# Kernel optimization log

Measured on AMD Instinct MI355X. Metric: run time of the kernel, lower is better.

The kernel has to match this reference:

```python
import jax, jax.numpy as jnp
import numpy as np

N_NODES = 50000
EPS_NORM = 1e-12
EPS_ENT = 1e-8

def _l2norm(x):
    # torch.nn.functional.normalize: x / clamp(||x||, min=1e-12)
    n = jnp.sqrt(jnp.sum(x * x, axis=-1, keepdims=True))
    return x / jnp.maximum(n, EPS_NORM)

def _layer(hidden, src, dst, edge_type, multi_emb, proto_emb):
    # hidden: [N,H]; multi_emb: [R,P,H]; proto_emb: [P,H]
    inp_j = hidden[src]                          # [E,H] gather
    rel_basis = multi_emb[edge_type]             # [E,P,H] gather
    sims = jnp.einsum('eh,ph->ep', _l2norm(inp_j), _l2norm(proto_emb))  # cosine sim [E,P]
    proto_proba = jax.nn.softmax(sims, axis=1)   # [E,P]
    msg = jnp.einsum('ep,eph->eh', proto_proba, rel_basis)              # [E,H]
    ent = -jnp.sum(proto_proba * jnp.log(proto_proba + EPS_ENT), axis=1)  # [E]
    logits = -ent
    # scatter_softmax over destination index
    seg_max = jax.ops.segment_max(logits, dst, num_segments=N_NODES)
    ex = jnp.exp(logits - seg_max[dst])
    denom = jax.ops.segment_sum(ex, dst, num_segments=N_NODES)
    attn = ex / denom[dst]                       # [E]
    out = jax.ops.segment_sum(attn[:, None] * msg, dst, num_segments=N_NODES)  # [N,H]
    return out

def setup_inputs() -> dict:
    key = jax.random.key(0)
    ks = jax.random.split(key, 6)
    E = 800000
    H, R, P, L = 128, 18, 18, 3  # num_layers=4 -> 3 NBFCluttr layers
    edge_index = jax.random.randint(ks[0], (2, E), 0, N_NODES, dtype=jnp.int64) if jax.config.read('jax_enable_x64') else jax.random.randint(ks[0], (2, E), 0, N_NODES, dtype=jnp.int32)
    edge_type = jax.random.randint(ks[1], (E,), 0, R, dtype=edge_index.dtype)
    tail_indices = jax.random.randint(ks[2], (1024,), 0, N_NODES, dtype=edge_index.dtype)
    multi_embeddings = jax.random.uniform(ks[3], (L, R, P, H), dtype=jnp.float32)
    proto_embeddings = jax.random.uniform(ks[4], (L, P, H), dtype=jnp.float32)
    source_embedding = jax.random.uniform(ks[5], (H,), dtype=jnp.float32)
    return {"edge_index": edge_index, "edge_type": edge_type, "tail_indices": tail_indices,
            "multi_embeddings": multi_embeddings, "proto_embeddings": proto_embeddings,
            "source_embedding": source_embedding}

def reference(edge_index, edge_type, tail_indices, multi_embeddings, proto_embeddings, source_embedding):
    src, dst = edge_index[0], edge_index[1]
    H = source_embedding.shape[0]
    # boundary condition: source node gets source_embedding, rest zero
    hidden = jnp.zeros((N_NODES, H), dtype=source_embedding.dtype).at[0].set(source_embedding)
    L = multi_embeddings.shape[0]
    for l in range(L):  # small fixed loop over structurally distinct layers
        hidden = _layer(hidden, src, dst, edge_type, multi_embeddings[l], proto_embeddings[l])
    # apply_classifier, eval_mode=True, use_mlp_classifier=False -> cosine sims to last layer prototypes
    out_emb = hidden[tail_indices]               # [B,H]
    sims = jnp.einsum('nh,ph->np', _l2norm(out_emb), _l2norm(proto_embeddings[-1]))
    return sims  # gumbel_softmax_sample with eval_mode=True returns logits unchanged
```

## Files before the change

### kernel.cpp

```cpp
#include <hip/hip_runtime.h>
#include <hip/hip_bf16.h>


#define N_NODES 50000
#define H 128
#define P 18
#define RP 324
#define KPAD 352
#define K0PAD 64
#define ELLW 64
#define NPART 8
#define NODES_PER_PART 6250

typedef _Float16 half8 __attribute__((ext_vector_type(8)));
typedef float floatx4 __attribute__((ext_vector_type(4)));

__global__ __launch_bounds__(256) void zero_u32_kernel(unsigned* p, int n) {
  int i = blockIdx.x * 256 + threadIdx.x;
  if (i < n) p[i] = 0u;
}

__global__ __launch_bounds__(256) void ell_kernel(const int* __restrict__ src,
                                                  const int* __restrict__ dst,
                                                  const int* __restrict__ etype,
                                                  unsigned* __restrict__ cur,
                                                  unsigned* __restrict__ ep, int E) {
  int part = blockIdx.x & (NPART - 1);
  int i = (blockIdx.x >> 3) * 256 + threadIdx.x;
  if (i >= E) return;
  int d = dst[i];
  int lo = part * NODES_PER_PART;
  if (d < lo || d >= lo + NODES_PER_PART) return;
  unsigned pos = atomicAdd(&cur[d], 1u);
  if (pos < ELLW)
    ep[(size_t)d * ELLW + pos] = (unsigned)src[i] | ((unsigned)etype[i] << 20);
}

__global__ __launch_bounds__(64) void protoq0_kernel(const float* __restrict__ proto,
                                                     const float* __restrict__ semb,
                                                     float* __restrict__ pN,
                                                     float* __restrict__ q0r) {
  int row = blockIdx.x, l = threadIdx.x;
  if (row < 54) {
    float a = proto[row * H + l], b = proto[row * H + 64 + l];
    float ss = a * a + b * b;
    for (int m = 32; m > 0; m >>= 1) ss += __shfl_xor(ss, m, 64);
    float inv = 1.f / fmaxf(sqrtf(ss), 1e-12f);
    pN[row * H + l] = a * inv;
    pN[row * H + 64 + l] = b * inv;
    return;
  }
  float s0 = semb[l], s1 = semb[l + 64];
  float ss = s0 * s0 + s1 * s1;
  float dot[P];
#pragma unroll
  for (int p = 0; p < P; p++) {
    float a = proto[p * H + l], b = proto[p * H + 64 + l];
    float rn = a * a + b * b;
    for (int m = 32; m > 0; m >>= 1) rn += __shfl_xor(rn, m, 64);
    float rinv = 1.f / fmaxf(sqrtf(rn), 1e-12f);
    dot[p] = (s0 * a + s1 * b) * rinv;
  }
  for (int m = 1; m <= 32; m <<= 1) {
    ss += __shfl_xor(ss, m, 64);
#pragma unroll
    for (int p = 0; p < P; p++) dot[p] += __shfl_xor(dot[p], m, 64);
  }
  float inv = 1.f / fmaxf(sqrtf(ss), 1e-12f);
  float sum = 0.f;
#pragma unroll
  for (int p = 0; p < P; p++) {
    dot[p] = __expf(dot[p] * inv - 1.f);
    sum += dot[p];
  }
  float isum = 1.f / sum, ent = 0.f;
#pragma unroll
  for (int p = 0; p < P; p++) {
    dot[p] *= isum;
    ent -= dot[p] * __logf(dot[p] + 1e-8f);
  }
  float w = __expf(-ent);
  if (l < P) q0r[l] = w * dot[l];
}

__global__ __launch_bounds__(256) void bprep_kernel(const float* __restrict__ multi,
                                                    const float* __restrict__ q0r,
                                                    _Float16* __restrict__ Btg,
                                                    _Float16* __restrict__ Btl0) {
  int idx = blockIdx.x * 256 + threadIdx.x;
  if (idx < 2 * H * KPAD) {
    int l = idx / (H * KPAD), rem = idx - l * (H * KPAD);
    int h = rem / KPAD, k = rem - h * KPAD;
    const float* B = multi + (size_t)(l + 1) * RP * H;
    Btg[idx] = (k < RP) ? (_Float16)B[k * H + h] : (_Float16)0.f;
    return;
  }
  int idx2 = idx - 2 * H * KPAD;
  if (idx2 >= H * K0PAD) return;
  int h = idx2 >> 6, k = idx2 & 63;
  float pr = 1.f / 18.f, ent = 0.f;
#pragma unroll
  for (int p = 0; p < P; p++) ent -= pr * __logf(pr + 1e-8f);
  float qc = __expf(-ent) * pr;
  float v = 0.f;
  if (k < P) {
#pragma unroll
    for (int p = 0; p < P; p++) v += qc * multi[(k * P + p) * H + h];
  } else if (k < 2 * P) {
    int r = k - P;
#pragma unroll
    for (int p = 0; p < P; p++) v += (q0r[p] - qc) * multi[(r * P + p) * H + h];
  }
  Btl0[h * K0PAD + k] = (_Float16)v;
}

__global__ __launch_bounds__(256) void hist_kernel(const unsigned* __restrict__ ep,
                                                   const unsigned* __restrict__ cur,
                                                   _Float16* __restrict__ M, int n) {
  int wave = threadIdx.x >> 6, lane = threadIdx.x & 63;
  int nd = blockIdx.x * 4 + wave;
  if (nd >= n) return;
  int cnt = (int)cur[nd];
  if (cnt > ELLW) cnt = ELLW;
  bool a = lane < cnt;
  unsigned pk = a ? ep[(size_t)nd * ELLW + lane] : 0xFFFFFFFFu;
  int r = (int)(pk >> 20);
  unsigned long long zm = __ballot(a && (pk & 0xFFFFFu) == 0u);
  float creg = 0.f, creg0 = 0.f;
#pragma unroll
  for (int rr = 0; rr < P; rr++) {
    unsigned long long m = __ballot(a && (r == rr));
    if (lane == rr) {
      creg = (float)__popcll(m);
      creg0 = (float)__popcll(m & zm);
    }
  }
  int slx = (lane >= P && lane < 2 * P) ? lane - P : 0;
  float v0 = __shfl(creg0, slx, 64);
  float val = (lane < P) ? creg : ((lane < 2 * P) ? v0 : 0.f);
  M[(size_t)nd * K0PAD + lane] = (_Float16)val;
}

__global__ __launch_bounds__(256) void scatter_kernel(const unsigned* __restrict__ ep,
                                                      const unsigned* __restrict__ cur,
                                                      const float* __restrict__ q,
                                                      const int* __restrict__ tl,
                                                      _Float16* __restrict__ M, int n) {
  __shared__ float sl[4][3 * RP];
  int wave = threadIdx.x >> 6, lane = threadIdx.x & 63;
  int t = blockIdx.x * 4 + wave;
  float* s0 = sl[wave];
  for (int i = lane; i < 3 * RP; i += 64) s0[i] = 0.f;
  int sub = lane / 18;
  int j = lane - sub * 18;
  bool act = (sub < 3) && (t < n);
  int cnt = 0;
  size_t b = 0;
  if (t < n) {
    int nd = tl ? tl[t] : t;
    b = (size_t)nd * ELLW;
    cnt = (int)cur[nd];
    if (cnt > ELLW) cnt = ELLW;
  }
  float* ms = s0 + (sub < 3 ? sub : 0) * RP;
  for (int it = 0; it < cnt; it += 9) {
    bool a0 = act && (it + sub < cnt);
    bool a1 = act && (it + 3 + sub < cnt);
    bool a2 = act && (it + 6 + sub < cnt);
    unsigned pk0 = 0, pk1 = 0, pk2 = 0;
    if (a0) pk0 = ep[b + it + sub];
    if (a1) pk1 = ep[b + it + 3 + sub];
    if (a2) pk2 = ep[b + it + 6 + sub];
    float q0 = 0.f, q1 = 0.f, q2 = 0.f;
    if (a0) q0 = q[(size_t)(pk0 & 0xFFFFFu) * P + j];
    if (a1) q1 = q[(size_t)(pk1 & 0xFFFFFu) * P + j];
    if (a2) q2 = q[(size_t)(pk2 & 0xFFFFFu) * P + j];
    if (a0) ms[(pk0 >> 20) * P + j] += q0;
    if (a1) ms[(pk1 >> 20) * P + j] += q1;
    if (a2) ms[(pk2 >> 20) * P + j] += q2;
  }
  if (t < n) {
    for (int k = lane; k < RP; k += 64)
      M[(size_t)t * KPAD + k] = (_Float16)(s0[k] + s0[RP + k] + s0[2 * RP + k]);
    for (int k = RP + lane; k < KPAD; k += 64) M[(size_t)t * KPAD + k] = (_Float16)0.f;
  }
}

template <int MODE>
__global__ __launch_bounds__(256) void gemm_kernel(const _Float16* __restrict__ M,
                                                   const _Float16* __restrict__ Bt,
                                                   const float* __restrict__ pN,
                                                   float* __restrict__ q_out, int n,
                                                   int kpad) {
  __shared__ float smem_f[64 * 132];
  _Float16* As = (_Float16*)smem_f;
  _Float16* Bs = (_Float16*)(smem_f + 1024);
  int tid = threadIdx.x;
  int wave = tid >> 6, lane = tid & 63;
  int m15 = lane & 15, quad = lane >> 4;
  int n0 = blockIdx.x * 64;
  floatx4 acc[4][2] = {};

  __shared__ float pns[4 * P * 36];
  for (int i = tid; i < 4 * P * 32; i += 256) {
    int s = i / (P * 32), r = i - s * (P * 32);
    int p = r >> 5, kk = r & 31;
    pns[s * (P * 36) + p * 36 + kk] = pN[p * H + s * 32 + kk];
  }

  for (int kt = 0; kt < (kpad >> 5); kt++) {
    int k0 = kt * 32;
    __syncthreads();
    {
      int row = tid >> 2, kc = (tid & 3) * 8;
      int gr = n0 + row;
      half8 v = {};
      if (gr < n) v = *(const half8*)(M + (size_t)gr * kpad + k0 + kc);
      *(half8*)(As + row * 32 + kc) = v;
    }
    {
      int col = tid >> 1, kc = (tid & 1) * 16;
      const _Float16* srcp = Bt + (size_t)col * kpad + k0 + kc;
      *(half8*)(Bs + col * 32 + kc) = *(const half8*)srcp;
      *(half8*)(Bs + col * 32 + kc + 8) = *(const half8*)(srcp + 8);
    }
    __syncthreads();
    half8 bfrag0 = *(const half8*)(Bs + (wave * 32 + m15) * 32 + quad * 8);
    half8 bfrag1 = *(const half8*)(Bs + (wave * 32 + 16 + m15) * 32 + quad * 8);
#pragma unroll
    for (int mt = 0; mt < 4; mt++) {
      half8 afrag = *(const half8*)(As + (mt * 16 + m15) * 32 + quad * 8);
      acc[mt][0] = __builtin_amdgcn_mfma_f32_16x16x32_f16(afrag, bfrag0, acc[mt][0], 0, 0, 0);
      acc[mt][1] = __builtin_amdgcn_mfma_f32_16x16x32_f16(afrag, bfrag1, acc[mt][1], 0, 0, 0);
    }
  }
  __syncthreads();
#pragma unroll
  for (int mt = 0; mt < 4; mt++)
#pragma unroll
    for (int c = 0; c < 2; c++)
#pragma unroll
      for (int reg = 0; reg < 4; reg++)
        smem_f[(mt * 16 + quad * 4 + reg) * 132 + wave * 32 + c * 16 + m15] = acc[mt][c][reg];
  __syncthreads();
  int node = tid >> 2, sub = tid & 3;
  int gnode = n0 + node;
  const float* trow = smem_f + node * 132 + sub * 32;
  const float* ps = pns + sub * (P * 36);
  float ss = 0.f;
  float dot[P];
#pragma unroll
  for (int p = 0; p < P; p++) dot[p] = 0.f;
#pragma unroll
  for (int k4 = 0; k4 < 8; k4++) {
    float4 y = *(const float4*)(trow + k4 * 4);
    ss += y.x * y.x + y.y * y.y + y.z * y.z + y.w * y.w;
#pragma unroll
    for (int p = 0; p < P; p++) {
      float4 b = *(const float4*)(ps + p * 36 + k4 * 4);
      dot[p] += y.x * b.x + y.y * b.y + y.z * b.z + y.w * b.w;
    }
  }
  for (int m = 1; m <= 2; m <<= 1) {
    ss += __shfl_xor(ss, m, 64);
#pragma unroll
    for (int p = 0; p < P; p++) dot[p] += __shfl_xor(dot[p], m, 64);
  }
  if (gnode < n) {
    float inv = 1.f / fmaxf(sqrtf(ss), 1e-12f);
    if (MODE == 1) {
      for (int p = sub; p < P; p += 4) q_out[(size_t)gnode * P + p] = dot[p] * inv;
    } else {
      float sum = 0.f;
#pragma unroll
      for (int p = 0; p < P; p++) {
        dot[p] = __expf(dot[p] * inv - 1.f);
        sum += dot[p];
      }
      float isum = 1.f / sum, ent = 0.f;
#pragma unroll
      for (int p = 0; p < P; p++) {
        dot[p] *= isum;
        ent -= dot[p] * __logf(dot[p] + 1e-8f);
      }
      float w = __expf(-ent);
      for (int p = sub; p < P; p += 4) q_out[(size_t)gnode * P + p] = w * dot[p];
    }
  }
}

extern "C" void kernel_launch(void* const* d_in, const int* in_sizes, int n_in,
                              void* d_out, int out_size, void* d_ws, size_t ws_size,
                              hipStream_t stream) {
  const int* eidx = (const int*)d_in[0];
  int E = in_sizes[0] / 2;
  const int* src = eidx;
  const int* dst = eidx + E;
  const int* etype = (const int*)d_in[1];
  const int* tails = (const int*)d_in[2];
  int T = in_sizes[2];
  const float* multi = (const float*)d_in[3];
  const float* proto = (const float*)d_in[4];
  const float* semb = (const float*)d_in[5];
  float* out = (float*)d_out;

  char* w = (char*)d_ws;
  auto alloc = [&](size_t bytes) {
    char* p = w;
    w += (bytes + 255) & ~(size_t)255;
    return p;
  };
  float* q = (float*)alloc((size_t)N_NODES * P * 4);
  float* q0r = (float*)alloc((size_t)P * 4);
  float* pNs = (float*)alloc((size_t)3 * P * H * 4);
  _Float16* Mg = (_Float16*)alloc((size_t)N_NODES * KPAD * 2);
  _Float16* Btg = (_Float16*)alloc((size_t)2 * H * KPAD * 2);
  _Float16* Btl0 = (_Float16*)alloc((size_t)H * K0PAD * 2);
  unsigned* cur = (unsigned*)alloc((size_t)N_NODES * 4);
  unsigned* ep = (unsigned*)alloc((size_t)N_NODES * ELLW * 4);

  int nb = (N_NODES + 255) / 256;
  int eb = (E + 255) / 256;

  zero_u32_kernel<<<nb, 256, 0, stream>>>(cur, N_NODES);
  ell_kernel<<<eb * NPART, 256, 0, stream>>>(src, dst, etype, cur, ep, E);

  protoq0_kernel<<<55, 64, 0, stream>>>(proto, semb, pNs, q0r);
  bprep_kernel<<<(2 * H * KPAD + H * K0PAD + 255) / 256, 256, 0, stream>>>(multi, q0r, Btg,
                                                                           Btl0);

  hist_kernel<<<(N_NODES + 3) / 4, 256, 0, stream>>>(ep, cur, Mg, N_NODES);
  gemm_kernel<0><<<(N_NODES + 63) / 64, 256, 0, stream>>>(Mg, Btl0, pNs + (size_t)1 * P * H, q,
                                                          N_NODES, K0PAD);

  scatter_kernel<<<(N_NODES + 3) / 4, 256, 0, stream>>>(ep, cur, q, nullptr, Mg, N_NODES);
  gemm_kernel<0><<<(N_NODES + 63) / 64, 256, 0, stream>>>(Mg, Btg, pNs + (size_t)2 * P * H, q,
                                                          N_NODES, KPAD);

  scatter_kernel<<<(T + 3) / 4, 256, 0, stream>>>(ep, cur, q, tails, Mg, T);
  gemm_kernel<1><<<(T + 63) / 64, 256, 0, stream>>>(Mg, Btg + (size_t)H * KPAD,
                                                    pNs + (size_t)2 * P * H, out, T, KPAD);
}
```

Baseline: 241.8 us.

## Fuse histogram into first GEMM, fold zeroing into prep, store q as fp16

The per-node relation histogram is now computed directly inside the layer-0 GEMM into shared memory, so the separate hist kernel and its round trip through the global M buffer go away. Zeroing of the edge counters moves into the bprep kernel, removing a launch. The per-node probability vector q is stored as fp16, halving the bytes gathered in the scatter kernel. The trade-off is lower precision on q and more per-block work in the first GEMM.

```diff
diff --git a/kernel.cpp b/kernel.cpp
--- a/kernel.cpp
+++ b/kernel.cpp
@@ -14,11 +14,6 @@
 
 typedef _Float16 half8 __attribute__((ext_vector_type(8)));
 typedef float floatx4 __attribute__((ext_vector_type(4)));
-
-__global__ __launch_bounds__(256) void zero_u32_kernel(unsigned* p, int n) {
-  int i = blockIdx.x * 256 + threadIdx.x;
-  if (i < n) p[i] = 0u;
-}
 
 __global__ __launch_bounds__(256) void ell_kernel(const int* __restrict__ src,
                                                   const int* __restrict__ dst,
@@ -86,8 +81,10 @@
 __global__ __launch_bounds__(256) void bprep_kernel(const float* __restrict__ multi,
                                                     const float* __restrict__ q0r,
                                                     _Float16* __restrict__ Btg,
-                                                    _Float16* __restrict__ Btl0) {
+                                                    _Float16* __restrict__ Btl0,
+                                                    unsigned* __restrict__ cur) {
   int idx = blockIdx.x * 256 + threadIdx.x;
+  if (idx < N_NODES) cur[idx] = 0u;
   if (idx < 2 * H * KPAD) {
     int l = idx / (H * KPAD), rem = idx - l * (H * KPAD);
     int h = rem / KPAD, k = rem - h * KPAD;
@@ -114,36 +111,9 @@
   Btl0[h * K0PAD + k] = (_Float16)v;
 }
 
-__global__ __launch_bounds__(256) void hist_kernel(const unsigned* __restrict__ ep,
-                                                   const unsigned* __restrict__ cur,
-                                                   _Float16* __restrict__ M, int n) {
-  int wave = threadIdx.x >> 6, lane = threadIdx.x & 63;
-  int nd = blockIdx.x * 4 + wave;
-  if (nd >= n) return;
-  int cnt = (int)cur[nd];
-  if (cnt > ELLW) cnt = ELLW;
-  bool a = lane < cnt;
-  unsigned pk = a ? ep[(size_t)nd * ELLW + lane] : 0xFFFFFFFFu;
-  int r = (int)(pk >> 20);
-  unsigned long long zm = __ballot(a && (pk & 0xFFFFFu) == 0u);
-  float creg = 0.f, creg0 = 0.f;
-#pragma unroll
-  for (int rr = 0; rr < P; rr++) {
-    unsigned long long m = __ballot(a && (r == rr));
-    if (lane == rr) {
-      creg = (float)__popcll(m);
-      creg0 = (float)__popcll(m & zm);
-    }
-  }
-  int slx = (lane >= P && lane < 2 * P) ? lane - P : 0;
-  float v0 = __shfl(creg0, slx, 64);
-  float val = (lane < P) ? creg : ((lane < 2 * P) ? v0 : 0.f);
-  M[(size_t)nd * K0PAD + lane] = (_Float16)val;
-}
-
 __global__ __launch_bounds__(256) void scatter_kernel(const unsigned* __restrict__ ep,
                                                       const unsigned* __restrict__ cur,
-                                                      const float* __restrict__ q,
+                                                      const _Float16* __restrict__ q,
                                                       const int* __restrict__ tl,
                                                       _Float16* __restrict__ M, int n) {
   __shared__ float sl[4][3 * RP];
@@ -172,9 +142,9 @@
     if (a1) pk1 = ep[b + it + 3 + sub];
     if (a2) pk2 = ep[b + it + 6 + sub];
     float q0 = 0.f, q1 = 0.f, q2 = 0.f;
-    if (a0) q0 = q[(size_t)(pk0 & 0xFFFFFu) * P + j];
-    if (a1) q1 = q[(size_t)(pk1 & 0xFFFFFu) * P + j];
-    if (a2) q2 = q[(size_t)(pk2 & 0xFFFFFu) * P + j];
+    if (a0) q0 = (float)q[(size_t)(pk0 & 0xFFFFFu) * P + j];
+    if (a1) q1 = (float)q[(size_t)(pk1 & 0xFFFFFu) * P + j];
+    if (a2) q2 = (float)q[(size_t)(pk2 & 0xFFFFFu) * P + j];
     if (a0) ms[(pk0 >> 20) * P + j] += q0;
     if (a1) ms[(pk1 >> 20) * P + j] += q1;
     if (a2) ms[(pk2 >> 20) * P + j] += q2;
@@ -190,17 +160,20 @@
 __global__ __launch_bounds__(256) void gemm_kernel(const _Float16* __restrict__ M,
                                                    const _Float16* __restrict__ Bt,
                                                    const float* __restrict__ pN,
-                                                   float* __restrict__ q_out, int n,
-                                                   int kpad) {
+                                                   void* __restrict__ out_ptr, int n,
+                                                   int kpad,
+                                                   const unsigned* __restrict__ ep,
+                                                   const unsigned* __restrict__ cur) {
   __shared__ float smem_f[64 * 132];
-  _Float16* As = (_Float16*)smem_f;
-  _Float16* Bs = (_Float16*)(smem_f + 1024);
   int tid = threadIdx.x;
   int wave = tid >> 6, lane = tid & 63;
   int m15 = lane & 15, quad = lane >> 4;
   int n0 = blockIdx.x * 64;
   floatx4 acc[4][2] = {};
 
+  _Float16* As = (_Float16*)smem_f;
+  _Float16* Bs = (_Float16*)(smem_f + (MODE == 2 ? 2048 : 1024));
+
   __shared__ float pns[4 * P * 36];
   for (int i = tid; i < 4 * P * 32; i += 256) {
     int s = i / (P * 32), r = i - s * (P * 32);
@@ -208,10 +181,40 @@
     pns[s * (P * 36) + p * 36 + kk] = pN[p * H + s * 32 + kk];
   }
 
+  if (MODE == 2) {
+    for (int i = 0; i < 16; i++) {
+      int node = wave * 16 + i;
+      int gnode = n0 + node;
+      int cnt = 0;
+      if (gnode < n) {
+        cnt = (int)cur[gnode];
+        if (cnt > ELLW) cnt = ELLW;
+      }
+      bool a = lane < cnt;
+      unsigned pk = a ? ep[(size_t)gnode * ELLW + lane] : 0xFFFFFFFFu;
+      int r = (int)(pk >> 20);
+      unsigned long long zm = __ballot(a && (pk & 0xFFFFFu) == 0u);
+      float creg = 0.f, creg0 = 0.f;
+#pragma unroll
+      for (int rr = 0; rr < P; rr++) {
+        unsigned long long m = __ballot(a && (r == rr));
+        if (lane == rr) {
+          creg = (float)__popcll(m);
+          creg0 = (float)__popcll(m & zm);
+        }
+      }
+      int slx = (lane >= P && lane < 2 * P) ? lane - P : 0;
+      float v0 = __shfl(creg0, slx, 64);
+      float val = (lane < P) ? creg : ((lane < 2 * P) ? v0 : 0.f);
+      As[node * 64 + lane] = (_Float16)val;
+    }
+  }
+  __syncthreads();
+
   for (int kt = 0; kt < (kpad >> 5); kt++) {
     int k0 = kt * 32;
-    __syncthreads();
-    {
+    if (kt) __syncthreads();
+    if (MODE != 2) {
       int row = tid >> 2, kc = (tid & 3) * 8;
       int gr = n0 + row;
       half8 v = {};
@@ -229,7 +232,11 @@
     half8 bfrag1 = *(const half8*)(Bs + (wave * 32 + 16 + m15) * 32 + quad * 8);
 #pragma unroll
     for (int mt = 0; mt < 4; mt++) {
-      half8 afrag = *(const half8*)(As + (mt * 16 + m15) * 32 + quad * 8);
+      half8 afrag;
+      if (MODE == 2)
+        afrag = *(const half8*)(As + (mt * 16 + m15) * 64 + k0 + quad * 8);
+      else
+        afrag = *(const half8*)(As + (mt * 16 + m15) * 32 + quad * 8);
       acc[mt][0] = __builtin_amdgcn_mfma_f32_16x16x32_f16(afrag, bfrag0, acc[mt][0], 0, 0, 0);
       acc[mt][1] = __builtin_amdgcn_mfma_f32_16x16x32_f16(afrag, bfrag1, acc[mt][1], 0, 0, 0);
     }
@@ -269,7 +276,8 @@
   if (gnode < n) {
     float inv = 1.f / fmaxf(sqrtf(ss), 1e-12f);
     if (MODE == 1) {
-      for (int p = sub; p < P; p += 4) q_out[(size_t)gnode * P + p] = dot[p] * inv;
+      float* outp = (float*)out_ptr;
+      for (int p = sub; p < P; p += 4) outp[(size_t)gnode * P + p] = dot[p] * inv;
     } else {
       float sum = 0.f;
 #pragma unroll
@@ -284,7 +292,8 @@
         ent -= dot[p] * __logf(dot[p] + 1e-8f);
       }
       float w = __expf(-ent);
-      for (int p = sub; p < P; p += 4) q_out[(size_t)gnode * P + p] = w * dot[p];
+      _Float16* qp = (_Float16*)out_ptr;
+      for (int p = sub; p < P; p += 4) qp[(size_t)gnode * P + p] = (_Float16)(w * dot[p]);
     }
   }
 }
@@ -310,7 +319,7 @@
     w += (bytes + 255) & ~(size_t)255;
     return p;
   };
-  float* q = (float*)alloc((size_t)N_NODES * P * 4);
+  _Float16* q = (_Float16*)alloc((size_t)N_NODES * P * 2);
   float* q0r = (float*)alloc((size_t)P * 4);
   float* pNs = (float*)alloc((size_t)3 * P * H * 4);
   _Float16* Mg = (_Float16*)alloc((size_t)N_NODES * KPAD * 2);
@@ -319,25 +328,22 @@
   unsigned* cur = (unsigned*)alloc((size_t)N_NODES * 4);
   unsigned* ep = (unsigned*)alloc((size_t)N_NODES * ELLW * 4);
 
-  int nb = (N_NODES + 255) / 256;
   int eb = (E + 255) / 256;
-
-  zero_u32_kernel<<<nb, 256, 0, stream>>>(cur, N_NODES);
-  ell_kernel<<<eb * NPART, 256, 0, stream>>>(src, dst, etype, cur, ep, E);
 
   protoq0_kernel<<<55, 64, 0, stream>>>(proto, semb, pNs, q0r);
   bprep_kernel<<<(2 * H * KPAD + H * K0PAD + 255) / 256, 256, 0, stream>>>(multi, q0r, Btg,
-                                                                           Btl0);
-
-  hist_kernel<<<(N_NODES + 3) / 4, 256, 0, stream>>>(ep, cur, Mg, N_NODES);
-  gemm_kernel<0><<<(N_NODES + 63) / 64, 256, 0, stream>>>(Mg, Btl0, pNs + (size_t)1 * P * H, q,
-                                                          N_NODES, K0PAD);
+                                                                           Btl0, cur);
+
+  ell_kernel<<<eb * NPART, 256, 0, stream>>>(src, dst, etype, cur, ep, E);
+
+  gemm_kernel<2><<<(N_NODES + 63) / 64, 256, 0, stream>>>(
+      nullptr, Btl0, pNs + (size_t)1 * P * H, q, N_NODES, K0PAD, ep, cur);
 
   scatter_kernel<<<(N_NODES + 3) / 4, 256, 0, stream>>>(ep, cur, q, nullptr, Mg, N_NODES);
-  gemm_kernel<0><<<(N_NODES + 63) / 64, 256, 0, stream>>>(Mg, Btg, pNs + (size_t)2 * P * H, q,
-                                                          N_NODES, KPAD);
+  gemm_kernel<0><<<(N_NODES + 63) / 64, 256, 0, stream>>>(
+      Mg, Btg, pNs + (size_t)2 * P * H, q, N_NODES, KPAD, nullptr, nullptr);
 
   scatter_kernel<<<(T + 3) / 4, 256, 0, stream>>>(ep, cur, q, tails, Mg, T);
-  gemm_kernel<1><<<(T + 63) / 64, 256, 0, stream>>>(Mg, Btg + (size_t)H * KPAD,
-                                                    pNs + (size_t)2 * P * H, out, T, KPAD);
-}
+  gemm_kernel<1><<<(T + 63) / 64, 256, 0, stream>>>(
+      Mg, Btg + (size_t)H * KPAD, pNs + (size_t)2 * P * H, out, T, KPAD, nullptr, nullptr);
+}
```

Result: slower. 256.0 us (+5.8%).
